# Performance work log

Hardware: AMD Instinct MI355X
Metric: run time of the kernel (lower is better)

Reference implementation:

```python
import jax, jax.numpy as jnp
import numpy as np

N_EXPERTS = 16
TOP_K = 2
D_MODEL = 1024
D_FF = 1024
D_FF_SHARED = 2048
T_TOKENS = 4096


def setup_inputs() -> dict:
    key = jax.random.key(0)
    ks = jax.random.split(key, 7)
    s = 0.02
    return {
        "hidden_states": jax.random.normal(ks[0], (T_TOKENS, D_MODEL), jnp.float32),
        "gate_weight": jax.random.normal(ks[1], (N_EXPERTS, D_MODEL), jnp.float32) * s,
        "expert_gate_up": jax.random.normal(ks[2], (N_EXPERTS, 2 * D_FF, D_MODEL), jnp.float32) * s,
        "expert_down": jax.random.normal(ks[3], (N_EXPERTS, D_MODEL, D_FF), jnp.float32) * s,
        "shared_gate_up": jax.random.normal(ks[4], (2 * D_FF_SHARED, D_MODEL), jnp.float32) * s,
        "shared_down": jax.random.normal(ks[5], (D_MODEL, D_FF_SHARED), jnp.float32) * s,
        "shared_expert_gate_weight": jax.random.normal(ks[6], (1, D_MODEL), jnp.float32) * s,
    }


def _moe_forward(x, gate_weight, expert_gate_up, expert_down):
    T = x.shape[0]
    E = gate_weight.shape[0]
    # Router: top-k over logits, softmax over the selected logits (fp32)
    router_logits = x @ gate_weight.T                      # [T, E]
    topk_logits, topk_ids = jax.lax.top_k(router_logits, TOP_K)
    topk_weights = jax.nn.softmax(topk_logits.astype(jnp.float32), axis=-1)
    # Dense combine matrix C[t, e] = routing weight of expert e for token t
    combine = jnp.zeros((T, E), jnp.float32).at[
        jnp.arange(T)[:, None], topk_ids
    ].add(topk_weights)                                    # [T, E]

    # Scan over experts to avoid materializing [E, T, d]
    def body(acc, inputs):
        w_gu, w_d, c_e = inputs                            # [2F,d], [d,F], [T]
        gu = x @ w_gu.T                                    # [T, 2F]
        g, u = gu[:, :D_FF], gu[:, D_FF:]
        h = jax.nn.silu(g) * u                             # [T, F]
        acc = acc + c_e[:, None] * (h @ w_d.T)             # [T, d]
        return acc, None

    acc0 = jnp.zeros_like(x)
    moe_out, _ = jax.lax.scan(body, acc0, (expert_gate_up, expert_down, combine.T))
    return moe_out


def _shared_expert(x, shared_gate_up, shared_down, shared_expert_gate_weight):
    gu = x @ shared_gate_up.T                              # [T, 2Fs]
    mid = gu.shape[-1] // 2
    h = jax.nn.silu(gu[:, :mid]) * gu[:, mid:]
    out = h @ shared_down.T                                # [T, d]
    gate = jax.nn.sigmoid(x @ shared_expert_gate_weight.T)  # [T, 1]
    return out * gate


def reference(hidden_states, gate_weight, expert_gate_up, expert_down,
              shared_gate_up, shared_down, shared_expert_gate_weight):
    moe_out = _moe_forward(hidden_states, gate_weight, expert_gate_up, expert_down)
    shared_out = _shared_expert(hidden_states, shared_gate_up, shared_down,
                                shared_expert_gate_weight)
    return moe_out + shared_out
```

## Files before the change

### kernel.cpp

```cpp
#include <hip/hip_runtime.h>
#include <hip/hip_bf16.h>

#define T_TOKENS 4096
#define D_MODEL  1024
#define N_EXP    16
#define D_FF     1024
#define D_FF_SH  2048

typedef __attribute__((ext_vector_type(8))) short short8;
typedef __attribute__((ext_vector_type(4))) float float4v;

__device__ __forceinline__ short f2bf(float f) {
    union { float f; unsigned u; } c; c.f = f;
    unsigned u = c.u + 0x7fffu + ((c.u >> 16) & 1u);
    return (short)(u >> 16);
}

__device__ __forceinline__ void gload16(const void* g, void* l) {
    __builtin_amdgcn_global_load_lds(
        (const __attribute__((address_space(1))) void*)g,
        (__attribute__((address_space(3))) void*)l, 16, 0, 0);
}

__global__ __launch_bounds__(256) void convert_all_kernel(
    const float* __restrict__ s0, short* __restrict__ d0,
    const float* __restrict__ s1, short* __restrict__ d1,
    const float* __restrict__ s2, short* __restrict__ d2,
    const float* __restrict__ s3, short* __restrict__ d3) {
    int c = blockIdx.x * 256 + threadIdx.x;
    const float* s; short* d; int off;
    if      (c < 4194304) { s = s0; d = d0; off = c; }
    else if (c < 6291456) { s = s1; d = d1; off = c - 4194304; }
    else if (c < 6815744) { s = s2; d = d2; off = c - 6291456; }
    else                  { s = s3; d = d3; off = c - 6815744; }
    size_t i = (size_t)off * 8;
    float4 a = *(const float4*)(s + i);
    float4 b = *(const float4*)(s + i + 4);
    union { short sh[8]; int4 v; } p;
    p.sh[0] = f2bf(a.x); p.sh[1] = f2bf(a.y); p.sh[2] = f2bf(a.z); p.sh[3] = f2bf(a.w);
    p.sh[4] = f2bf(b.x); p.sh[5] = f2bf(b.y); p.sh[6] = f2bf(b.z); p.sh[7] = f2bf(b.w);
    *(int4*)(d + i) = p.v;
}

__global__ __launch_bounds__(256) void router_kernel(
    const float* __restrict__ x, const float* __restrict__ gw, const float* __restrict__ sgw,
    short* __restrict__ xb, int* __restrict__ topk_id, float* __restrict__ topk_w,
    float* __restrict__ gate, int* __restrict__ counts) {
    __shared__ float gwl[17 * 1024];
    int tid = threadIdx.x;
#pragma unroll
    for (int i = 0; i < 16; i++)
        *(float4*)&gwl[tid * 4 + i * 1024] = *(const float4*)&gw[tid * 4 + i * 1024];
    *(float4*)&gwl[16384 + tid * 4] = *(const float4*)&sgw[tid * 4];
    __syncthreads();

    int wave = tid >> 6, lane = tid & 63;
    int t0 = blockIdx.x * 16 + wave * 4;

    float acc[4][17];
#pragma unroll
    for (int tt = 0; tt < 4; tt++)
#pragma unroll
        for (int e = 0; e < 17; e++) acc[tt][e] = 0.f;

#pragma unroll
    for (int i = 0; i < 4; i++) {
        int d = lane * 4 + i * 256;
        float4 xv[4];
#pragma unroll
        for (int tt = 0; tt < 4; tt++) {
            xv[tt] = *(const float4*)&x[(size_t)(t0 + tt) * D_MODEL + d];
            union { short sh[4]; int2 v; } p;
            p.sh[0] = f2bf(xv[tt].x); p.sh[1] = f2bf(xv[tt].y);
            p.sh[2] = f2bf(xv[tt].z); p.sh[3] = f2bf(xv[tt].w);
            *(int2*)&xb[(size_t)(t0 + tt) * D_MODEL + d] = p.v;
        }
#pragma unroll
        for (int e = 0; e < 17; e++) {
            float4 g = *(const float4*)&gwl[e * 1024 + d];
#pragma unroll
            for (int tt = 0; tt < 4; tt++)
                acc[tt][e] += xv[tt].x * g.x + xv[tt].y * g.y + xv[tt].z * g.z + xv[tt].w * g.w;
        }
    }

#pragma unroll
    for (int tt = 0; tt < 4; tt++)
#pragma unroll
        for (int e = 0; e < 17; e++)
            for (int off = 32; off; off >>= 1) acc[tt][e] += __shfl_xor(acc[tt][e], off);

    if (lane == 0) {
#pragma unroll
        for (int tt = 0; tt < 4; tt++) {
            int t = t0 + tt;
            float v1 = -1e30f, v2 = -1e30f; int i1 = 0, i2 = 0;
#pragma unroll
            for (int e = 0; e < 16; e++) {
                float v = acc[tt][e];
                if (v > v1) { v2 = v1; i2 = i1; v1 = v; i1 = e; }
                else if (v > v2) { v2 = v; i2 = e; }
            }
            float e2 = expf(v2 - v1);
            float s = 1.f + e2;
            topk_id[t * 2] = i1; topk_id[t * 2 + 1] = i2;
            topk_w[t * 2] = 1.f / s; topk_w[t * 2 + 1] = e2 / s;
            gate[t] = 1.f / (1.f + expf(-acc[tt][16]));
            atomicAdd(&counts[i1], 1); atomicAdd(&counts[i2], 1);
        }
    }
}

__global__ void offsets_kernel(const int* __restrict__ counts, int* __restrict__ offsets,
                               int* __restrict__ cursor, int* __restrict__ tile_map,
                               int* __restrict__ n_tiles) {
    if (threadIdx.x == 0) {
        int off = 0, nt = 0;
        for (int e = 0; e < N_EXP; e++) {
            offsets[e] = off; cursor[e] = off;
            int c = counts[e];
            for (int r = 0; r < c; r += 256) tile_map[nt++] = (e << 16) | (r >> 8);
            off += c;
        }
        n_tiles[0] = nt;
    }
}

__global__ __launch_bounds__(256) void scatter_kernel(
    const int* __restrict__ topk_id, const float* __restrict__ topk_w,
    int* __restrict__ cursor, int* __restrict__ tok_list, float* __restrict__ tok_w,
    int* __restrict__ slot_of) {
    int t = blockIdx.x * 256 + threadIdx.x;
#pragma unroll
    for (int k = 0; k < 2; k++) {
        int e = topk_id[t * 2 + k];
        int pos = atomicAdd(&cursor[e], 1);
        tok_list[pos] = t;
        tok_w[pos] = topk_w[t * 2 + k];
        slot_of[t * 2 + k] = pos;
    }
}

__global__ __launch_bounds__(512, 2) void gemm1_kernel(
    const short* __restrict__ xb,
    const short* __restrict__ Wexp,
    const short* __restrict__ Wsh,
    short* __restrict__ Hexp,
    short* __restrict__ Hsh,
    const int* __restrict__ tok_list,
    const int* __restrict__ offsets, const int* __restrict__ counts,
    const int* __restrict__ tile_map, const int* __restrict__ n_tiles) {
    __shared__ char lds[65536];

    int nt = n_tiles[0];
    int total = nt * 8 + 256;

    int t = threadIdx.x;
    int wave = t >> 6, lane = t & 63;
    int wm = (wave & 3) * 64, wn = (wave >> 2) * 64;
    int fr = lane & 15, fk2 = (lane >> 4) * 16;
    int rA = t >> 2;
    int cq = (t & 3) * 8;
    int lo = t * 16;
    int erow = (lane >> 4) * 4;
    int ecol = lane & 15;

    for (int it = blockIdx.x; it < total; it += gridDim.x) {
        int count, row0, col0, dff;
        const int* idx = nullptr;
        const short* Wg; short* Hout;
        if (it < nt * 8) {
            int tm = tile_map[it >> 3];
            int e = tm >> 16; row0 = (tm & 0xffff) << 8;
            col0 = (it & 7) * 128;
            count = counts[e];
            int base = offsets[e];
            idx = tok_list + base;
            Wg = Wexp + (size_t)e * 2 * D_FF * D_MODEL;
            Hout = Hexp + (size_t)base * D_FF;
            dff = D_FF;
        } else {
            int s = it - nt * 8;
            row0 = (s >> 4) * 256; col0 = (s & 15) * 128;
            count = T_TOKENS;
            Wg = Wsh; Hout = Hsh; dff = D_FF_SH;
        }
        const short* Wu = Wg + (size_t)dff * D_MODEL;

        float4v accg[4][4], accu[4][4];
#pragma unroll
        for (int i = 0; i < 4; i++)
#pragma unroll
            for (int j = 0; j < 4; j++) { accg[i][j] = (float4v)0.f; accu[i][j] = (float4v)0.f; }

        int r0c = min(row0 + rA, count - 1);
        int r1c = min(row0 + rA + 128, count - 1);
        int g0 = idx ? idx[r0c] : r0c;
        int g1 = idx ? idx[r1c] : r1c;
        const short* aP0 = xb + (size_t)g0 * D_MODEL + cq;
        const short* aP1 = xb + (size_t)g1 * D_MODEL + cq;
        const short* bgP = Wg + (size_t)(col0 + rA) * D_MODEL + cq;
        const short* buP = Wu + (size_t)(col0 + rA) * D_MODEL + cq;

        __syncthreads();
        gload16(aP0, lds + lo);
        gload16(aP1, lds + 8192 + lo);
        gload16(bgP, lds + 16384 + lo);
        gload16(buP, lds + 24576 + lo);

        const int NK = D_MODEL / 32;
        for (int k = 0; k < NK; k++) {
            __syncthreads();
            if (k + 1 < NK) {
                int s = ((k + 1) & 1) * 32768;
                int off = (k + 1) * 32;
                gload16(aP0 + off, lds + s + lo);
                gload16(aP1 + off, lds + s + 8192 + lo);
                gload16(bgP + off, lds + s + 16384 + lo);
                gload16(buP + off, lds + s + 24576 + lo);
            }
            int sb = (k & 1) * 32768;
            short8 af[4], bgf[4], buf[4];
#pragma unroll
            for (int i = 0; i < 4; i++)
                af[i] = *(const short8*)(lds + sb + (wm + i * 16 + fr) * 64 + fk2);
#pragma unroll
            for (int j = 0; j < 4; j++) {
                bgf[j] = *(const short8*)(lds + sb + 16384 + (wn + j * 16 + fr) * 64 + fk2);
                buf[j] = *(const short8*)(lds + sb + 24576 + (wn + j * 16 + fr) * 64 + fk2);
            }
#pragma unroll
            for (int i = 0; i < 4; i++)
#pragma unroll
                for (int j = 0; j < 4; j++) {
                    accg[i][j] = __builtin_amdgcn_mfma_f32_16x16x32_bf16(af[i], bgf[j], accg[i][j], 0, 0, 0);
                    accu[i][j] = __builtin_amdgcn_mfma_f32_16x16x32_bf16(af[i], buf[j], accu[i][j], 0, 0, 0);
                }
        }

#pragma unroll
        for (int i = 0; i < 4; i++)
#pragma unroll
            for (int j = 0; j < 4; j++)
#pragma unroll
                for (int r = 0; r < 4; r++) {
                    int row = wm + i * 16 + erow + r;
                    if (row0 + row < count) {
                        float g = accg[i][j][r], u = accu[i][j][r];
                        float h = g / (1.f + expf(-g)) * u;
                        Hout[(size_t)(row0 + row) * dff + col0 + wn + j * 16 + ecol] = f2bf(h);
                    }
                }
    }
}

__global__ __launch_bounds__(512, 2) void gemm2_kernel(
    const short* __restrict__ Hexp, const short* __restrict__ Hsh,
    const short* __restrict__ Wdexp,
    const short* __restrict__ Wdsh,
    float* __restrict__ oslots,
    float* __restrict__ out,
    const float* __restrict__ tok_w, const float* __restrict__ gate,
    const int* __restrict__ offsets, const int* __restrict__ counts,
    const int* __restrict__ tile_map, const int* __restrict__ n_tiles) {
    __shared__ char lds[49152];

    int nt = n_tiles[0];
    int total = nt * 8 + 128;

    int t = threadIdx.x;
    int wave = t >> 6, lane = t & 63;
    int wm = (wave & 3) * 64, wn = (wave >> 2) * 64;
    int fr = lane & 15, fk2 = (lane >> 4) * 16;
    int rA = t >> 2;
    int cq = (t & 3) * 8;
    int lo = t * 16;
    int erow = (lane >> 4) * 4;
    int ecol = lane & 15;

    for (int it = blockIdx.x; it < total; it += gridDim.x) {
        int count, row0, col0, K, base;
        const short* Ab; const short* B;
        bool shared_part;
        if (it < nt * 8) {
            int tm = tile_map[it >> 3];
            int e = tm >> 16; row0 = (tm & 0xffff) << 8;
            col0 = (it & 7) * 128;
            count = counts[e]; base = offsets[e];
            Ab = Hexp + (size_t)base * D_FF; K = D_FF;
            B = Wdexp + (size_t)e * D_MODEL * D_FF;
            shared_part = false;
        } else {
            int s = it - nt * 8;
            row0 = (s >> 3) * 256; col0 = (s & 7) * 128;
            count = T_TOKENS; base = 0;
            Ab = Hsh; K = D_FF_SH; B = Wdsh; shared_part = true;
        }

        float4v acc[4][4];
#pragma unroll
        for (int i = 0; i < 4; i++)
#pragma unroll
            for (int j = 0; j < 4; j++) acc[i][j] = (float4v)0.f;

        int r0c = min(row0 + rA, count - 1);
        int r1c = min(row0 + rA + 128, count - 1);
        const short* aP0 = Ab + (size_t)r0c * K + cq;
        const short* aP1 = Ab + (size_t)r1c * K + cq;
        const short* bP  = B + (size_t)(col0 + rA) * K + cq;

        __syncthreads();
        gload16(aP0, lds + lo);
        gload16(aP1, lds + 8192 + lo);
        gload16(bP,  lds + 16384 + lo);

        const int NK = K / 32;
        for (int k = 0; k < NK; k++) {
            __syncthreads();
            if (k + 1 < NK) {
                int s = ((k + 1) & 1) * 24576;
                int off = (k + 1) * 32;
                gload16(aP0 + off, lds + s + lo);
                gload16(aP1 + off, lds + s + 8192 + lo);
                gload16(bP + off,  lds + s + 16384 + lo);
            }
            int sb = (k & 1) * 24576;
            short8 af[4], bf[4];
#pragma unroll
            for (int i = 0; i < 4; i++)
                af[i] = *(const short8*)(lds + sb + (wm + i * 16 + fr) * 64 + fk2);
#pragma unroll
            for (int j = 0; j < 4; j++)
                bf[j] = *(const short8*)(lds + sb + 16384 + (wn + j * 16 + fr) * 64 + fk2);
#pragma unroll
            for (int i = 0; i < 4; i++)
#pragma unroll
                for (int j = 0; j < 4; j++)
                    acc[i][j] = __builtin_amdgcn_mfma_f32_16x16x32_bf16(af[i], bf[j], acc[i][j], 0, 0, 0);
        }

#pragma unroll
        for (int i = 0; i < 4; i++)
#pragma unroll
            for (int j = 0; j < 4; j++)
#pragma unroll
                for (int r = 0; r < 4; r++) {
                    int row = wm + i * 16 + erow + r;
                    if (row0 + row < count) {
                        float v = acc[i][j][r];
                        int col = col0 + wn + j * 16 + ecol;
                        if (!shared_part) {
                            int slot = base + row0 + row;
                            oslots[(size_t)slot * D_MODEL + col] = tok_w[slot] * v;
                        } else {
                            out[(size_t)(row0 + row) * D_MODEL + col] = gate[row0 + row] * v;
                        }
                    }
                }
    }
}

__global__ __launch_bounds__(256) void combine_kernel(
    float* __restrict__ out, const float* __restrict__ oslots,
    const int* __restrict__ slot_of) {
    int t = blockIdx.x;
    int sA = slot_of[t * 2], sB = slot_of[t * 2 + 1];
    int d = threadIdx.x * 4;
    float4 o = *(float4*)&out[(size_t)t * D_MODEL + d];
    float4 a = *(const float4*)&oslots[(size_t)sA * D_MODEL + d];
    float4 b = *(const float4*)&oslots[(size_t)sB * D_MODEL + d];
    o.x += a.x + b.x; o.y += a.y + b.y; o.z += a.z + b.z; o.w += a.w + b.w;
    *(float4*)&out[(size_t)t * D_MODEL + d] = o;
}

extern "C" void kernel_launch(void* const* d_in, const int* in_sizes, int n_in,
                              void* d_out, int out_size, void* d_ws, size_t ws_size,
                              hipStream_t stream) {
    const float* x     = (const float*)d_in[0];
    const float* gw    = (const float*)d_in[1];
    const float* egu   = (const float*)d_in[2];
    const float* edown = (const float*)d_in[3];
    const float* sgu   = (const float*)d_in[4];
    const float* sdown = (const float*)d_in[5];
    const float* sgate = (const float*)d_in[6];
    float* out = (float*)d_out;
    char* ws = (char*)d_ws;

    const size_t XB_OFF     = 0;
    const size_t WGU_OFF    = XB_OFF     + (size_t)4096*1024*2;
    const size_t WDOWN_OFF  = WGU_OFF    + (size_t)16*2048*1024*2;
    const size_t WSGU_OFF   = WDOWN_OFF  + (size_t)16*1024*1024*2;
    const size_t WSDOWN_OFF = WSGU_OFF   + (size_t)4096*1024*2;
    const size_t HEXP_OFF   = WSDOWN_OFF + (size_t)1024*2048*2;
    const size_t HSH_OFF    = HEXP_OFF   + (size_t)8192*1024*2;
    const size_t OSLOT_OFF  = HSH_OFF    + (size_t)4096*2048*2;
    const size_t TID_OFF    = OSLOT_OFF  + (size_t)8192*1024*4;
    const size_t TW_OFF     = TID_OFF    + 4096*2*4;
    const size_t GATE_OFF   = TW_OFF     + 4096*2*4;
    const size_t TOKL_OFF   = GATE_OFF   + 4096*4;
    const size_t TOKW_OFF   = TOKL_OFF   + 8192*4;
    const size_t SLOT_OFF   = TOKW_OFF   + 8192*4;
    const size_t CNT_OFF    = SLOT_OFF   + 8192*4;
    const size_t OFFS_OFF   = CNT_OFF    + 256;
    const size_t CUR_OFF    = OFFS_OFF   + 256;
    const size_t TMAP_OFF   = CUR_OFF    + 256;
    const size_t NT_OFF     = TMAP_OFF   + 512;

    short* xb      = (short*)(ws + XB_OFF);
    short* wgu_b   = (short*)(ws + WGU_OFF);
    short* wdown_b = (short*)(ws + WDOWN_OFF);
    short* wsgu_b  = (short*)(ws + WSGU_OFF);
    short* wsdn_b  = (short*)(ws + WSDOWN_OFF);
    short* h_exp   = (short*)(ws + HEXP_OFF);
    short* h_sh    = (short*)(ws + HSH_OFF);
    float* oslots  = (float*)(ws + OSLOT_OFF);
    int*   topk_id = (int*)(ws + TID_OFF);
    float* topk_w  = (float*)(ws + TW_OFF);
    float* gate    = (float*)(ws + GATE_OFF);
    int*   tok_l   = (int*)(ws + TOKL_OFF);
    float* tok_w   = (float*)(ws + TOKW_OFF);
    int*   slot_of = (int*)(ws + SLOT_OFF);
    int*   counts  = (int*)(ws + CNT_OFF);
    int*   offsets = (int*)(ws + OFFS_OFF);
    int*   cursor  = (int*)(ws + CUR_OFF);
    int*   tmap    = (int*)(ws + TMAP_OFF);
    int*   ntiles  = (int*)(ws + NT_OFF);

    hipMemsetAsync(counts, 0, 64, stream);

    convert_all_kernel<<<27648, 256, 0, stream>>>(egu, wgu_b, edown, wdown_b,
                                                  sgu, wsgu_b, sdown, wsdn_b);
    router_kernel<<<256, 256, 0, stream>>>(x, gw, sgate, xb, topk_id, topk_w, gate, counts);
    offsets_kernel<<<1, 64, 0, stream>>>(counts, offsets, cursor, tmap, ntiles);
    scatter_kernel<<<T_TOKENS / 256, 256, 0, stream>>>(topk_id, topk_w, cursor, tok_l, tok_w, slot_of);

    gemm1_kernel<<<512, 512, 0, stream>>>(
        xb, wgu_b, wsgu_b, h_exp, h_sh, tok_l, offsets, counts, tmap, ntiles);

    gemm2_kernel<<<384, 512, 0, stream>>>(
        h_exp, h_sh, wdown_b, wsdn_b, oslots, out, tok_w, gate, offsets, counts, tmap, ntiles);

    combine_kernel<<<T_TOKENS, 256, 0, stream>>>(out, oslots, slot_of);
}
```

Measured before the change: 618.3 us.

## Fuse expert combine into down-projection via float atomics on zeroed output

The per-slot output buffer and the separate combine kernel are removed. gemm2 now atomically adds its weighted results directly into the output, which is zeroed up front, and it launches more blocks with a higher occupancy hint. Fast exp intrinsics replace expf in the router and the SiLU. This avoids writing and rereading a large fp32 intermediate and saves one launch, at the cost of many global float atomics and a nondeterministic summation order.

```diff
diff --git a/kernel.cpp b/kernel.cpp
--- a/kernel.cpp
+++ b/kernel.cpp
@@ -101,11 +101,11 @@
                 if (v > v1) { v2 = v1; i2 = i1; v1 = v; i1 = e; }
                 else if (v > v2) { v2 = v; i2 = e; }
             }
-            float e2 = expf(v2 - v1);
+            float e2 = __expf(v2 - v1);
             float s = 1.f + e2;
             topk_id[t * 2] = i1; topk_id[t * 2 + 1] = i2;
             topk_w[t * 2] = 1.f / s; topk_w[t * 2 + 1] = e2 / s;
-            gate[t] = 1.f / (1.f + expf(-acc[tt][16]));
+            gate[t] = 1.f / (1.f + __expf(-acc[tt][16]));
             atomicAdd(&counts[i1], 1); atomicAdd(&counts[i2], 1);
         }
     }
@@ -128,8 +128,7 @@
 
 __global__ __launch_bounds__(256) void scatter_kernel(
     const int* __restrict__ topk_id, const float* __restrict__ topk_w,
-    int* __restrict__ cursor, int* __restrict__ tok_list, float* __restrict__ tok_w,
-    int* __restrict__ slot_of) {
+    int* __restrict__ cursor, int* __restrict__ tok_list, float* __restrict__ tok_w) {
     int t = blockIdx.x * 256 + threadIdx.x;
 #pragma unroll
     for (int k = 0; k < 2; k++) {
@@ -137,7 +136,6 @@
         int pos = atomicAdd(&cursor[e], 1);
         tok_list[pos] = t;
         tok_w[pos] = topk_w[t * 2 + k];
-        slot_of[t * 2 + k] = pos;
     }
 }
 
@@ -247,19 +245,19 @@
                     int row = wm + i * 16 + erow + r;
                     if (row0 + row < count) {
                         float g = accg[i][j][r], u = accu[i][j][r];
-                        float h = g / (1.f + expf(-g)) * u;
+                        float h = g / (1.f + __expf(-g)) * u;
                         Hout[(size_t)(row0 + row) * dff + col0 + wn + j * 16 + ecol] = f2bf(h);
                     }
                 }
     }
 }
 
-__global__ __launch_bounds__(512, 2) void gemm2_kernel(
+__global__ __launch_bounds__(512, 6) void gemm2_kernel(
     const short* __restrict__ Hexp, const short* __restrict__ Hsh,
     const short* __restrict__ Wdexp,
     const short* __restrict__ Wdsh,
-    float* __restrict__ oslots,
     float* __restrict__ out,
+    const int* __restrict__ tok_list,
     const float* __restrict__ tok_w, const float* __restrict__ gate,
     const int* __restrict__ offsets, const int* __restrict__ counts,
     const int* __restrict__ tile_map, const int* __restrict__ n_tiles) {
@@ -351,26 +349,15 @@
                         int col = col0 + wn + j * 16 + ecol;
                         if (!shared_part) {
                             int slot = base + row0 + row;
-                            oslots[(size_t)slot * D_MODEL + col] = tok_w[slot] * v;
+                            int tok = tok_list[slot];
+                            atomicAdd(&out[(size_t)tok * D_MODEL + col], tok_w[slot] * v);
                         } else {
-                            out[(size_t)(row0 + row) * D_MODEL + col] = gate[row0 + row] * v;
+                            atomicAdd(&out[(size_t)(row0 + row) * D_MODEL + col],
+                                      gate[row0 + row] * v);
                         }
                     }
                 }
     }
-}
-
-__global__ __launch_bounds__(256) void combine_kernel(
-    float* __restrict__ out, const float* __restrict__ oslots,
-    const int* __restrict__ slot_of) {
-    int t = blockIdx.x;
-    int sA = slot_of[t * 2], sB = slot_of[t * 2 + 1];
-    int d = threadIdx.x * 4;
-    float4 o = *(float4*)&out[(size_t)t * D_MODEL + d];
-    float4 a = *(const float4*)&oslots[(size_t)sA * D_MODEL + d];
-    float4 b = *(const float4*)&oslots[(size_t)sB * D_MODEL + d];
-    o.x += a.x + b.x; o.y += a.y + b.y; o.z += a.z + b.z; o.w += a.w + b.w;
-    *(float4*)&out[(size_t)t * D_MODEL + d] = o;
 }
 
 extern "C" void kernel_launch(void* const* d_in, const int* in_sizes, int n_in,
@@ -393,14 +380,12 @@
     const size_t WSDOWN_OFF = WSGU_OFF   + (size_t)4096*1024*2;
     const size_t HEXP_OFF   = WSDOWN_OFF + (size_t)1024*2048*2;
     const size_t HSH_OFF    = HEXP_OFF   + (size_t)8192*1024*2;
-    const size_t OSLOT_OFF  = HSH_OFF    + (size_t)4096*2048*2;
-    const size_t TID_OFF    = OSLOT_OFF  + (size_t)8192*1024*4;
+    const size_t TID_OFF    = HSH_OFF    + (size_t)4096*2048*2;
     const size_t TW_OFF     = TID_OFF    + 4096*2*4;
     const size_t GATE_OFF   = TW_OFF     + 4096*2*4;
     const size_t TOKL_OFF   = GATE_OFF   + 4096*4;
     const size_t TOKW_OFF   = TOKL_OFF   + 8192*4;
-    const size_t SLOT_OFF   = TOKW_OFF   + 8192*4;
-    const size_t CNT_OFF    = SLOT_OFF   + 8192*4;
+    const size_t CNT_OFF    = TOKW_OFF   + 8192*4;
     const size_t OFFS_OFF   = CNT_OFF    + 256;
     const size_t CUR_OFF    = OFFS_OFF   + 256;
     const size_t TMAP_OFF   = CUR_OFF    + 256;
@@ -413,13 +398,11 @@
     short* wsdn_b  = (short*)(ws + WSDOWN_OFF);
     short* h_exp   = (short*)(ws + HEXP_OFF);
     short* h_sh    = (short*)(ws + HSH_OFF);
-    float* oslots  = (float*)(ws + OSLOT_OFF);
     int*   topk_id = (int*)(ws + TID_OFF);
     float* topk_w  = (float*)(ws + TW_OFF);
     float* gate    = (float*)(ws + GATE_OFF);
     int*   tok_l   = (int*)(ws + TOKL_OFF);
     float* tok_w   = (float*)(ws + TOKW_OFF);
-    int*   slot_of = (int*)(ws + SLOT_OFF);
     int*   counts  = (int*)(ws + CNT_OFF);
     int*   offsets = (int*)(ws + OFFS_OFF);
     int*   cursor  = (int*)(ws + CUR_OFF);
@@ -427,18 +410,17 @@
     int*   ntiles  = (int*)(ws + NT_OFF);
 
     hipMemsetAsync(counts, 0, 64, stream);
+    hipMemsetAsync(out, 0, (size_t)T_TOKENS * D_MODEL * 4, stream);
 
     convert_all_kernel<<<27648, 256, 0, stream>>>(egu, wgu_b, edown, wdown_b,
                                                   sgu, wsgu_b, sdown, wsdn_b);
     router_kernel<<<256, 256, 0, stream>>>(x, gw, sgate, xb, topk_id, topk_w, gate, counts);
     offsets_kernel<<<1, 64, 0, stream>>>(counts, offsets, cursor, tmap, ntiles);
-    scatter_kernel<<<T_TOKENS / 256, 256, 0, stream>>>(topk_id, topk_w, cursor, tok_l, tok_w, slot_of);
+    scatter_kernel<<<T_TOKENS / 256, 256, 0, stream>>>(topk_id, topk_w, cursor, tok_l, tok_w);
 
     gemm1_kernel<<<512, 512, 0, stream>>>(
         xb, wgu_b, wsgu_b, h_exp, h_sh, tok_l, offsets, counts, tmap, ntiles);
 
-    gemm2_kernel<<<384, 512, 0, stream>>>(
-        h_exp, h_sh, wdown_b, wsdn_b, oslots, out, tok_w, gate, offsets, counts, tmap, ntiles);
-
-    combine_kernel<<<T_TOKENS, 256, 0, stream>>>(out, oslots, slot_of);
-}
+    gemm2_kernel<<<768, 512, 0, stream>>>(
+        h_exp, h_sh, wdown_b, wsdn_b, out, tok_l, tok_w, gate, offsets, counts, tmap, ntiles);
+}
```

New measurement: 855.9 us. 38.4% more time.
